# Optimization experiments

Measured on AMD Instinct MI355X. Metric: run time of the kernel, lower is better.

The kernel has to match this reference:

```python
import jax, jax.numpy as jnp
import numpy as np

C = 256   # descriptor_dim
H = 4     # num_heads
D = C // H  # head_dim = 64
B, N = 8, 2048


def _conv1x1(x, w, b):
    # 1x1 Conv1d == per-position linear over channels: x [B,C,N], w [O,C], b [O]
    return jnp.einsum('oc,bcn->bon', w, x) + b[None, :, None]


def setup_inputs() -> dict:
    key = jax.random.key(0)
    ks = jax.random.split(key, 11)
    s = 1.0 / np.sqrt(C)
    return {
        'query': jax.random.normal(ks[0], (B, C, N), dtype=jnp.float32),
        'key':   jax.random.normal(ks[1], (B, C, N), dtype=jnp.float32),
        'value': jax.random.normal(ks[2], (B, C, N), dtype=jnp.float32),
        'wq': jax.random.normal(ks[3], (C, C), dtype=jnp.float32) * s,
        'bq': jax.random.normal(ks[4], (C,), dtype=jnp.float32) * s,
        'wk': jax.random.normal(ks[5], (C, C), dtype=jnp.float32) * s,
        'bk': jax.random.normal(ks[6], (C,), dtype=jnp.float32) * s,
        'wv': jax.random.normal(ks[7], (C, C), dtype=jnp.float32) * s,
        'bv': jax.random.normal(ks[8], (C,), dtype=jnp.float32) * s,
        'wm': jax.random.normal(ks[9], (C, C), dtype=jnp.float32) * s,
        'bm': jax.random.normal(ks[10], (C,), dtype=jnp.float32) * s,
    }


def reference(query, key, value, wq, bq, wk, bk, wv, bv, wm, bm):
    b = query.shape[0]
    # project then view channels as (head_dim, num_heads) -- matches torch .view order
    q = _conv1x1(query, wq, bq).reshape(b, D, H, -1)   # [B,D,H,N]
    k = _conv1x1(key,   wk, bk).reshape(b, D, H, -1)   # [B,D,H,M]
    v = _conv1x1(value, wv, bv).reshape(b, D, H, -1)   # [B,D,H,M]
    scores = jnp.einsum('bdhn,bdhm->bhnm', q, k) / (D ** 0.5)
    probs = jax.nn.softmax(scores, axis=-1)            # [B,H,N,M]
    out = jnp.einsum('bhnm,bdhm->bdhn', probs, v)      # [B,D,H,N]
    out = out.reshape(b, D * H, -1)                    # [B,C,N]
    return _conv1x1(out, wm, bm)
```

## Files before the change

kernel.cpp:

```cpp
#include <hip/hip_runtime.h>
#include <hip/hip_bf16.h>

typedef float f32x4 __attribute__((ext_vector_type(4)));
typedef float f32x16 __attribute__((ext_vector_type(16)));
typedef __bf16 bf16x8 __attribute__((ext_vector_type(8)));
typedef __bf16 bf16x4 __attribute__((ext_vector_type(4)));
typedef unsigned int uint2v __attribute__((ext_vector_type(2)));
typedef unsigned int u32;

constexpr int B_ = 8, C_ = 256, N_ = 2048, H_ = 4, D_ = 64;
constexpr int BH_ = B_ * H_;
constexpr size_t PER_ = (size_t)BH_ * N_ * D_;
constexpr float LOG2E = 1.44269504088896340736f;

static __device__ __forceinline__ float fast_exp2(float x) {
#if __has_builtin(__builtin_amdgcn_exp2f)
  return __builtin_amdgcn_exp2f(x);
#else
  return exp2f(x);
#endif
}

static __device__ __forceinline__ void* swz(void* base, int row, int cb) {
  return (char*)base + row * 128 + (cb ^ ((row & 7) << 4));
}
static __device__ __forceinline__ const void* swz(const void* base, int row, int cb) {
  return (const char*)base + row * 128 + (cb ^ ((row & 7) << 4));
}

static __device__ __forceinline__ void gload16(void* lds, const void* g) {
  __builtin_amdgcn_global_load_lds(
      (const __attribute__((address_space(1))) u32*)g,
      (__attribute__((address_space(3))) u32*)lds, 16, 0, 0);
}

struct W4 {
  const float* s0; const float* s1; const float* s2; const float* s3;
  __bf16* d0; __bf16* d1; __bf16* d2; __bf16* d3;
};

__global__ __launch_bounds__(256) void wcvt_kernel(W4 p) {
  const int m = blockIdx.y;
  const float* src = m == 0 ? p.s0 : m == 1 ? p.s1 : m == 2 ? p.s2 : p.s3;
  __bf16* dst = m == 0 ? p.d0 : m == 1 ? p.d1 : m == 2 ? p.d2 : p.d3;
  const int f = blockIdx.x * 256 + threadIdx.x;
  const int o_blk = f >> 9;
  const int ks = (f >> 6) & 7;
  const int lane = f & 63;
  const int row = o_blk * 16 + (lane & 15);
  const int kbase = ks * 32 + (lane >> 4) * 8;
  bf16x8 v;
  if (m == 3) {
    for (int e = 0; e < 8; e++) {
      const int k = kbase + e;
      const int c = ((k & 63) << 2) | (k >> 6);
      v[e] = (__bf16)src[row * 256 + c];
    }
  } else {
    const int srow = ((row & 63) << 2) | (row >> 6);
    const float* s = src + srow * 256 + kbase;
    float4 a = *(const float4*)s;
    float4 b = *(const float4*)(s + 4);
    v[0] = (__bf16)a.x; v[1] = (__bf16)a.y; v[2] = (__bf16)a.z; v[3] = (__bf16)a.w;
    v[4] = (__bf16)b.x; v[5] = (__bf16)b.y; v[6] = (__bf16)b.z; v[7] = (__bf16)b.w;
  }
  *(bf16x8*)&dst[(size_t)f * 8] = v;
}

__global__ __launch_bounds__(256) void qkv_fused_kernel(
    const float* __restrict__ xq, const float* __restrict__ xk,
    const float* __restrict__ xv, const __bf16* __restrict__ wfq,
    const __bf16* __restrict__ wfk, const __bf16* __restrict__ wfv,
    const float* __restrict__ bq, const float* __restrict__ bk,
    const float* __restrict__ bv, __bf16* __restrict__ oq,
    char* __restrict__ oksw, char* __restrict__ ovsw) {
  __shared__ __bf16 xlds[64][264];

  const int m = blockIdx.x >> 8;
  int inner = blockIdx.x & 255;
  inner = (inner & 7) * 32 + (inner >> 3);
  const int b = inner >> 5, nb = inner & 31;
  const int n0 = nb * 64;

  const float* xf = m == 0 ? xq : m == 1 ? xk : xv;
  const __bf16* wf = m == 0 ? wfq : m == 1 ? wfk : wfv;
  const float* bias = m == 0 ? bq : m == 1 ? bk : bv;
  const float scale = m == 0 ? 0.125f * LOG2E : 1.0f;

  const int t = threadIdx.x;
  {
    const int kl = t & 15;
    const int nl = (t >> 4) * 4;
    const float* src = xf + (size_t)b * C_ * N_ + n0 + nl;
    for (int kp = 0; kp < 8; kp++) {
      const int k = kp * 32 + kl * 2;
      float4 f0 = *(const float4*)(src + (size_t)k * N_);
      float4 f1 = *(const float4*)(src + (size_t)(k + 1) * N_);
      union { __bf16 h[2]; u32 u; } c0, c1, c2, c3;
      c0.h[0] = (__bf16)f0.x; c0.h[1] = (__bf16)f1.x;
      c1.h[0] = (__bf16)f0.y; c1.h[1] = (__bf16)f1.y;
      c2.h[0] = (__bf16)f0.z; c2.h[1] = (__bf16)f1.z;
      c3.h[0] = (__bf16)f0.w; c3.h[1] = (__bf16)f1.w;
      *(u32*)&xlds[nl + 0][k] = c0.u;
      *(u32*)&xlds[nl + 1][k] = c1.u;
      *(u32*)&xlds[nl + 2][k] = c2.u;
      *(u32*)&xlds[nl + 3][k] = c3.u;
    }
  }
  __syncthreads();

  const int lane = t & 63, wvv = t >> 6;
  const int wm = wvv >> 1, wn = wvv & 1;
  const int l15 = lane & 15, lg = lane >> 4;

  f32x4 acc[8][2] = {};

  for (int ks = 0; ks < 8; ks++) {
    bf16x8 bfr[2];
    for (int ni = 0; ni < 2; ni++)
      bfr[ni] = *(const bf16x8*)&xlds[wn * 32 + ni * 16 + l15][ks * 32 + lg * 8];
    for (int mi = 0; mi < 8; mi++) {
      bf16x8 af = *(const bf16x8*)&wf[(((size_t)(wm * 8 + mi) * 8 + ks) * 64 + lane) * 8];
      acc[mi][0] = __builtin_amdgcn_mfma_f32_16x16x32_bf16(af, bfr[0], acc[mi][0], 0, 0, 0);
      acc[mi][1] = __builtin_amdgcn_mfma_f32_16x16x32_bf16(af, bfr[1], acc[mi][1], 0, 0, 0);
    }
  }

  for (int mi = 0; mi < 8; mi++) {
    const int h = wm * 2 + (mi >> 2);
    const int d0 = (mi & 3) * 16 + 4 * lg;
    for (int ni = 0; ni < 2; ni++) {
      const int n = n0 + wn * 32 + ni * 16 + l15;
      const size_t tbase = ((size_t)(b * H_ + h) * (N_ / 64) + (n >> 6)) * 8192;
      if (m == 0) {
        bf16x4 o4;
        for (int r = 0; r < 4; r++)
          o4[r] = (__bf16)((acc[mi][ni][r] + bias[((d0 + r) << 2) | h]) * scale);
        *(bf16x4*)&oq[((size_t)(b * H_ + h) * N_ + n) * D_ + d0] = o4;
      } else if (m == 1) {
        bf16x4 o4;
        for (int r = 0; r < 4; r++)
          o4[r] = (__bf16)(acc[mi][ni][r] + bias[((d0 + r) << 2) | h]);
        *(bf16x4*)swz(oksw + tbase, n & 63, 2 * d0) = o4;
      } else {
        for (int r = 0; r < 4; r++)
          *(__bf16*)swz(ovsw + tbase, d0 + r, 2 * (n & 63)) =
              (__bf16)(acc[mi][ni][r] + bias[((d0 + r) << 2) | h]);
      }
    }
  }
}

template <int NS>
__global__ __launch_bounds__(256) void final_proj_kernel(
    const __bf16* __restrict__ p, const float* __restrict__ lb,
    const __bf16* __restrict__ wf, const float* __restrict__ bias,
    float* __restrict__ out) {
  const int bid = blockIdx.x;
  const int wid = (bid & 7) * 128 + (bid >> 3);
  const int o_t = wid & 3;
  const int nb = (wid >> 2) & 31;
  const int b = wid >> 7;
  const int o0 = o_t * 64, n0 = nb * 64;
  const int t = threadIdx.x, lane = t & 63;
  const int wvv = t >> 6, wm = wvv >> 1, wn = wvv & 1;
  const int l15 = lane & 15, lg = lane >> 4;
  const int nbase = n0 + wn * 32 + l15;

  float inv[2][4];
  if constexpr (NS > 1) {
    for (int ni = 0; ni < 2; ni++)
      for (int h = 0; h < 4; h++) {
        const size_t bhn = (size_t)(b * H_ + h) * N_ + nbase + ni * 16;
        float ls = 0.f;
#pragma unroll
        for (int u = 0; u < NS; u++) ls += lb[(size_t)u * BH_ * N_ + bhn];
        inv[ni][h] = 1.f / ls;
      }
  }

  f32x4 acc[2][2] = {};

  for (int ks = 0; ks < 8; ks++) {
    bf16x8 af[2];
    for (int mi = 0; mi < 2; mi++)
      af[mi] = *(const bf16x8*)&wf[(((size_t)(o_t * 4 + wm * 2 + mi) * 8 + ks) * 64 + lane) * 8];
    bf16x8 bfr[2];
    const int h = ks >> 1;
    const size_t bh = (size_t)(b * H_ + h);
    const int d0 = (ks & 1) * 32 + lg * 8;
    for (int ni = 0; ni < 2; ni++) {
      const size_t off = (bh * N_ + nbase + ni * 16) * D_ + d0;
      if constexpr (NS == 1) {
        bfr[ni] = *(const bf16x8*)&p[off];
      } else {
        float s8[8] = {};
#pragma unroll
        for (int u = 0; u < NS; u++) {
          bf16x8 a = *(const bf16x8*)&p[(size_t)u * PER_ + off];
#pragma unroll
          for (int e = 0; e < 8; e++) s8[e] += (float)a[e];
        }
        const float iv = inv[ni][h];
        bf16x8 r;
#pragma unroll
        for (int e = 0; e < 8; e++) r[e] = (__bf16)(s8[e] * iv);
        bfr[ni] = r;
      }
    }
    for (int mi = 0; mi < 2; mi++)
      for (int ni = 0; ni < 2; ni++)
        acc[mi][ni] = __builtin_amdgcn_mfma_f32_16x16x32_bf16(
            af[mi], bfr[ni], acc[mi][ni], 0, 0, 0);
  }

  for (int mi = 0; mi < 2; mi++) {
    for (int r = 0; r < 4; r++) {
      const int och = o0 + wm * 32 + mi * 16 + 4 * lg + r;
      const float bv_ = bias[och];
      for (int ni = 0; ni < 2; ni++) {
        const int n = n0 + wn * 32 + ni * 16 + l15;
        out[((size_t)b * C_ + och) * N_ + n] = acc[mi][ni][r] + bv_;
      }
    }
  }
}

template <int SPLIT>
__global__ __launch_bounds__(512) void attn_kernel(
    const __bf16* __restrict__ qb, const char* __restrict__ kbsw,
    const char* __restrict__ vtsw, __bf16* __restrict__ pO,
    float* __restrict__ lbuf) {
  __shared__ char smem[32768];

  const int t = threadIdx.x, lane = t & 63, wv = t >> 6;
  const int l31 = lane & 31, hi = lane >> 5;

  const int bid = blockIdx.x;
  const int per_xcd = (256 * SPLIT) / 8;
  const int wid = (bid & 7) * per_xcd + (bid >> 3);
  const int bh = wid / (8 * SPLIT);
  const int rem = wid % (8 * SPLIT);
  const int qt = rem % 8;
  const int s = rem / 8;
  const int qn = qt * 256 + wv * 32;
  constexpr int NT = N_ / SPLIT / 64;
  const int jt0 = s * NT;

  const char* ktiles = kbsw + (size_t)bh * (N_ / 64) * 8192;
  const char* vtiles = vtsw + (size_t)bh * (N_ / 64) * 8192;

  const __bf16* qrow = qb + ((size_t)bh * N_ + qn + l31) * D_;
  bf16x8 qf[4];
#pragma unroll
  for (int i = 0; i < 4; i++) qf[i] = *(const bf16x8*)(qrow + i * 16 + hi * 8);

  auto stage = [&](int jt_g, int bb) {
    gload16(smem + bb * 8192 + t * 16, ktiles + (size_t)jt_g * 8192 + t * 16);
    gload16(smem + 16384 + bb * 8192 + t * 16,
            vtiles + (size_t)jt_g * 8192 + t * 16);
  };

  stage(jt0, 0);
  __syncthreads();

  f32x16 o0 = {}, o1 = {};
  float la0 = 0.f, la1 = 0.f, la2 = 0.f, la3 = 0.f;
  int cur = 0;

  for (int jt = 0; jt < NT; jt++) {
    if (jt + 1 < NT) stage(jt0 + jt + 1, cur ^ 1);
    const char* kc = smem + cur * 8192;
    const char* vc = smem + 16384 + cur * 8192;

    f32x16 s0 = {}, s1 = {};
    __builtin_amdgcn_s_setprio(1);
#pragma unroll
    for (int i = 0; i < 4; i++) {
      bf16x8 kf = *(const bf16x8*)swz(kc, l31, i * 32 + hi * 16);
      s0 = __builtin_amdgcn_mfma_f32_32x32x16_bf16(kf, qf[i], s0, 0, 0, 0);
    }
#pragma unroll
    for (int i = 0; i < 4; i++) {
      bf16x8 kf = *(const bf16x8*)swz(kc, 32 + l31, i * 32 + hi * 16);
      s1 = __builtin_amdgcn_mfma_f32_32x32x16_bf16(kf, qf[i], s1, 0, 0, 0);
    }
    __builtin_amdgcn_s_setprio(0);

#pragma unroll
    for (int sub = 0; sub < 2; sub++) {
      const f32x16 sv = sub ? s1 : s0;
      float pr[16];
#pragma unroll
      for (int r = 0; r < 16; r++) pr[r] = fast_exp2(sv[r]);
      la0 += pr[0] + pr[4] + pr[8] + pr[12];
      la1 += pr[1] + pr[5] + pr[9] + pr[13];
      la2 += pr[2] + pr[6] + pr[10] + pr[14];
      la3 += pr[3] + pr[7] + pr[11] + pr[15];
      unsigned w[8];
#pragma unroll
      for (int g = 0; g < 8; g++) {
        union { __bf16 h[2]; unsigned u; } cv;
        cv.h[0] = (__bf16)pr[2 * g];
        cv.h[1] = (__bf16)pr[2 * g + 1];
        w[g] = cv.u;
      }
      uint2v r0 = __builtin_amdgcn_permlane32_swap(w[0], w[2], false, false);
      uint2v r1 = __builtin_amdgcn_permlane32_swap(w[1], w[3], false, false);
      uint2v r2 = __builtin_amdgcn_permlane32_swap(w[4], w[6], false, false);
      uint2v r3 = __builtin_amdgcn_permlane32_swap(w[5], w[7], false, false);
      union { unsigned u[4]; bf16x8 v; } f0 = {{r0.x, r1.x, r0.y, r1.y}};
      union { unsigned u[4]; bf16x8 v; } f1 = {{r2.x, r3.x, r2.y, r3.y}};
      const int scb = sub * 64;
      __builtin_amdgcn_s_setprio(1);
      {
        bf16x8 vf = *(const bf16x8*)swz(vc, l31, scb + hi * 16);
        o0 = __builtin_amdgcn_mfma_f32_32x32x16_bf16(vf, f0.v, o0, 0, 0, 0);
        vf = *(const bf16x8*)swz(vc, l31, scb + 32 + hi * 16);
        o0 = __builtin_amdgcn_mfma_f32_32x32x16_bf16(vf, f1.v, o0, 0, 0, 0);
        vf = *(const bf16x8*)swz(vc, 32 + l31, scb + hi * 16);
        o1 = __builtin_amdgcn_mfma_f32_32x32x16_bf16(vf, f0.v, o1, 0, 0, 0);
        vf = *(const bf16x8*)swz(vc, 32 + l31, scb + 32 + hi * 16);
        o1 = __builtin_amdgcn_mfma_f32_32x32x16_bf16(vf, f1.v, o1, 0, 0, 0);
      }
      __builtin_amdgcn_s_setprio(0);
    }

    __syncthreads();
    cur ^= 1;
  }

  float la = la0 + la1 + la2 + la3;
  la += __shfl_xor(la, 32);
  const float scl = (SPLIT == 1) ? 1.f / la : 1.f;

  if constexpr (SPLIT > 1) {
    if (hi == 0)
      lbuf[(size_t)s * BH_ * N_ + (size_t)bh * N_ + qn + l31] = la;
  }

  char* ep = smem + wv * 4096;
#pragma unroll
  for (int dt = 0; dt < 2; dt++) {
    const f32x16 o = dt ? o1 : o0;
#pragma unroll
    for (int g = 0; g < 4; g++) {
      bf16x4 o4;
#pragma unroll
      for (int j = 0; j < 4; j++) o4[j] = (__bf16)(o[4 * g + j] * scl);
      *(bf16x4*)swz(ep, l31, dt * 64 + 16 * g + 8 * hi) = o4;
    }
  }
  asm volatile("" ::: "memory");
  {
    __bf16* dst = pO + (size_t)s * PER_ + ((size_t)bh * N_ + qn) * D_;
#pragma unroll
    for (int i = 0; i < 4; i++) {
      const int row = i * 8 + (lane >> 3);
      uint4 v = *(const uint4*)swz(ep, row, (lane & 7) * 16);
      *(uint4*)((char*)dst + i * 1024 + lane * 16) = v;
    }
  }
}

extern "C" void kernel_launch(void* const* d_in, const int* in_sizes, int n_in,
                              void* d_out, int out_size, void* d_ws,
                              size_t ws_size, hipStream_t stream) {
  const float* query = (const float*)d_in[0];
  const float* key_ = (const float*)d_in[1];
  const float* value = (const float*)d_in[2];
  const float* wq = (const float*)d_in[3];
  const float* bq = (const float*)d_in[4];
  const float* wk = (const float*)d_in[5];
  const float* bk = (const float*)d_in[6];
  const float* wv = (const float*)d_in[7];
  const float* bv = (const float*)d_in[8];
  const float* wm = (const float*)d_in[9];
  const float* bm = (const float*)d_in[10];

  __bf16* qb = (__bf16*)d_ws;
  char* kbsw = (char*)(qb + PER_);
  char* vtsw = kbsw + PER_ * 2;
  float* lbuf = (float*)(vtsw + PER_ * 2);
  __bf16* wfq = (__bf16*)(lbuf + 4 * BH_ * N_);
  __bf16* wfk = wfq + 65536;
  __bf16* wfv = wfk + 65536;
  __bf16* wfm = wfv + 65536;
  __bf16* p0 = wfm + 65536;

  const size_t fixed = (size_t)((char*)p0 - (char*)d_ws);
  const int ns = (ws_size >= fixed + 4 * PER_ * 2) ? 4
               : (ws_size >= fixed + 2 * PER_ * 2) ? 2 : 1;

  dim3 blk(256);
  W4 wp{wq, wk, wv, wm, wfq, wfk, wfv, wfm};
  wcvt_kernel<<<dim3(32, 4), blk, 0, stream>>>(wp);

  qkv_fused_kernel<<<768, blk, 0, stream>>>(query, key_, value, wfq, wfk, wfv,
                                            bq, bk, bv, qb, kbsw, vtsw);
  if (ns == 4) {
    attn_kernel<4><<<1024, dim3(512), 0, stream>>>(qb, kbsw, vtsw, p0, lbuf);
    final_proj_kernel<4><<<1024, blk, 0, stream>>>(p0, lbuf, wfm, bm,
                                                   (float*)d_out);
  } else if (ns == 2) {
    attn_kernel<2><<<512, dim3(512), 0, stream>>>(qb, kbsw, vtsw, p0, lbuf);
    final_proj_kernel<2><<<1024, blk, 0, stream>>>(p0, lbuf, wfm, bm,
                                                   (float*)d_out);
  } else {
    attn_kernel<1><<<256, dim3(512), 0, stream>>>(qb, kbsw, vtsw, p0, nullptr);
    final_proj_kernel<1><<<1024, blk, 0, stream>>>(p0, nullptr, wfm, bm,
                                                   (float*)d_out);
  }
}
```

Before: 117.8 us.

## Stage K/V swizzled tiles in LDS for coalesced stores; cap split-KV at two

The QKV projection kernel now writes the K and V swizzled tile images into shared memory first, then copies each 8 KB per-head tile to global memory with contiguous 16-byte stores. Before, it scattered 8-byte and 2-byte writes straight to global memory. This targets the uncoalesced global write traffic for K and V, at the cost of two extra barriers and LDS round trips. Separately, the 4-way split-KV attention path is removed, so at most a 2-way split is used. That changes the attention grid size and the reduction work in the final projection.

```diff
diff --git a/kernel.cpp b/kernel.cpp
--- a/kernel.cpp
+++ b/kernel.cpp
@@ -74,7 +74,10 @@
     const float* __restrict__ bq, const float* __restrict__ bk,
     const float* __restrict__ bv, __bf16* __restrict__ oq,
     char* __restrict__ oksw, char* __restrict__ ovsw) {
-  __shared__ __bf16 xlds[64][264];
+  __shared__ union {
+    __bf16 xlds[64][264];
+    char img[32768];
+  } sh;
 
   const int m = blockIdx.x >> 8;
   int inner = blockIdx.x & 255;
@@ -101,10 +104,10 @@
       c1.h[0] = (__bf16)f0.y; c1.h[1] = (__bf16)f1.y;
       c2.h[0] = (__bf16)f0.z; c2.h[1] = (__bf16)f1.z;
       c3.h[0] = (__bf16)f0.w; c3.h[1] = (__bf16)f1.w;
-      *(u32*)&xlds[nl + 0][k] = c0.u;
-      *(u32*)&xlds[nl + 1][k] = c1.u;
-      *(u32*)&xlds[nl + 2][k] = c2.u;
-      *(u32*)&xlds[nl + 3][k] = c3.u;
+      *(u32*)&sh.xlds[nl + 0][k] = c0.u;
+      *(u32*)&sh.xlds[nl + 1][k] = c1.u;
+      *(u32*)&sh.xlds[nl + 2][k] = c2.u;
+      *(u32*)&sh.xlds[nl + 3][k] = c3.u;
     }
   }
   __syncthreads();
@@ -118,7 +121,7 @@
   for (int ks = 0; ks < 8; ks++) {
     bf16x8 bfr[2];
     for (int ni = 0; ni < 2; ni++)
-      bfr[ni] = *(const bf16x8*)&xlds[wn * 32 + ni * 16 + l15][ks * 32 + lg * 8];
+      bfr[ni] = *(const bf16x8*)&sh.xlds[wn * 32 + ni * 16 + l15][ks * 32 + lg * 8];
     for (int mi = 0; mi < 8; mi++) {
       bf16x8 af = *(const bf16x8*)&wf[(((size_t)(wm * 8 + mi) * 8 + ks) * 64 + lane) * 8];
       acc[mi][0] = __builtin_amdgcn_mfma_f32_16x16x32_bf16(af, bfr[0], acc[mi][0], 0, 0, 0);
@@ -126,27 +129,46 @@
     }
   }
 
-  for (int mi = 0; mi < 8; mi++) {
-    const int h = wm * 2 + (mi >> 2);
-    const int d0 = (mi & 3) * 16 + 4 * lg;
-    for (int ni = 0; ni < 2; ni++) {
-      const int n = n0 + wn * 32 + ni * 16 + l15;
-      const size_t tbase = ((size_t)(b * H_ + h) * (N_ / 64) + (n >> 6)) * 8192;
-      if (m == 0) {
+  if (m == 0) {
+    for (int mi = 0; mi < 8; mi++) {
+      const int h = wm * 2 + (mi >> 2);
+      const int d0 = (mi & 3) * 16 + 4 * lg;
+      for (int ni = 0; ni < 2; ni++) {
+        const int n = n0 + wn * 32 + ni * 16 + l15;
         bf16x4 o4;
         for (int r = 0; r < 4; r++)
           o4[r] = (__bf16)((acc[mi][ni][r] + bias[((d0 + r) << 2) | h]) * scale);
         *(bf16x4*)&oq[((size_t)(b * H_ + h) * N_ + n) * D_ + d0] = o4;
-      } else if (m == 1) {
-        bf16x4 o4;
-        for (int r = 0; r < 4; r++)
-          o4[r] = (__bf16)(acc[mi][ni][r] + bias[((d0 + r) << 2) | h]);
-        *(bf16x4*)swz(oksw + tbase, n & 63, 2 * d0) = o4;
-      } else {
-        for (int r = 0; r < 4; r++)
-          *(__bf16*)swz(ovsw + tbase, d0 + r, 2 * (n & 63)) =
-              (__bf16)(acc[mi][ni][r] + bias[((d0 + r) << 2) | h]);
-      }
+      }
+    }
+  } else {
+    __syncthreads();
+    for (int mi = 0; mi < 8; mi++) {
+      const int h = wm * 2 + (mi >> 2);
+      const int d0 = (mi & 3) * 16 + 4 * lg;
+      char* himg = sh.img + h * 8192;
+      for (int ni = 0; ni < 2; ni++) {
+        const int nl = wn * 32 + ni * 16 + l15;
+        if (m == 1) {
+          bf16x4 o4;
+          for (int r = 0; r < 4; r++)
+            o4[r] = (__bf16)(acc[mi][ni][r] + bias[((d0 + r) << 2) | h]);
+          *(bf16x4*)swz(himg, nl, 2 * d0) = o4;
+        } else {
+          for (int r = 0; r < 4; r++)
+            *(__bf16*)swz(himg, d0 + r, 2 * nl) =
+                (__bf16)(acc[mi][ni][r] + bias[((d0 + r) << 2) | h]);
+        }
+      }
+    }
+    __syncthreads();
+    char* outt = (m == 1) ? oksw : ovsw;
+#pragma unroll
+    for (int h = 0; h < 4; h++) {
+      const size_t tb = ((size_t)(b * H_ + h) * (N_ / 64) + nb) * 8192;
+      *(uint4*)(outt + tb + t * 32) = *(const uint4*)(sh.img + h * 8192 + t * 32);
+      *(uint4*)(outt + tb + t * 32 + 16) =
+          *(const uint4*)(sh.img + h * 8192 + t * 32 + 16);
     }
   }
 }
@@ -382,15 +404,14 @@
   char* kbsw = (char*)(qb + PER_);
   char* vtsw = kbsw + PER_ * 2;
   float* lbuf = (float*)(vtsw + PER_ * 2);
-  __bf16* wfq = (__bf16*)(lbuf + 4 * BH_ * N_);
+  __bf16* wfq = (__bf16*)(lbuf + 2 * BH_ * N_);
   __bf16* wfk = wfq + 65536;
   __bf16* wfv = wfk + 65536;
   __bf16* wfm = wfv + 65536;
   __bf16* p0 = wfm + 65536;
 
   const size_t fixed = (size_t)((char*)p0 - (char*)d_ws);
-  const int ns = (ws_size >= fixed + 4 * PER_ * 2) ? 4
-               : (ws_size >= fixed + 2 * PER_ * 2) ? 2 : 1;
+  const int ns = (ws_size >= fixed + 2 * PER_ * 2) ? 2 : 1;
 
   dim3 blk(256);
   W4 wp{wq, wk, wv, wm, wfq, wfk, wfv, wfm};
@@ -398,11 +419,7 @@
 
   qkv_fused_kernel<<<768, blk, 0, stream>>>(query, key_, value, wfq, wfk, wfv,
                                             bq, bk, bv, qb, kbsw, vtsw);
-  if (ns == 4) {
-    attn_kernel<4><<<1024, dim3(512), 0, stream>>>(qb, kbsw, vtsw, p0, lbuf);
-    final_proj_kernel<4><<<1024, blk, 0, stream>>>(p0, lbuf, wfm, bm,
-                                                   (float*)d_out);
-  } else if (ns == 2) {
+  if (ns == 2) {
     attn_kernel<2><<<512, dim3(512), 0, stream>>>(qb, kbsw, vtsw, p0, lbuf);
     final_proj_kernel<2><<<1024, blk, 0, stream>>>(p0, lbuf, wfm, bm,
                                                    (float*)d_out);
```

Result: no change. 118.9 us (+0.9%).
